# Optimization experiments

Hardware: AMD Instinct MI355X
Metric: run time of the kernel (lower is better)

Reference implementation:

```python
import jax, jax.numpy as jnp
import numpy as np

DEPTH, SRC, TRG, B, H = 2, 32, 32, 64, 256


def setup_inputs() -> dict:
    key = jax.random.key(0)
    k0, k1, k2, k3 = jax.random.split(key, 4)
    return {
        "src": jax.random.normal(k0, (SRC, B, H), jnp.float32),
        "trg": jax.random.normal(k1, (TRG, B, H), jnp.float32),
        # xavier-normal-ish scaling for the recurrent / input weights
        "W": jax.random.normal(k2, (DEPTH, H, H), jnp.float32) * (1.0 / np.sqrt(H)),
        "U": jax.random.normal(k3, (DEPTH, 2 * H, H), jnp.float32) * (1.0 / np.sqrt(2 * H)),
        "b": jnp.zeros((DEPTH, H), jnp.float32),
    }


def _run_depth(xw, yw, U, b):
    """2D grid recurrence for one depth.
    xw, yw: [SRC, TRG, B, H] precomputed input projections (x_t @ W, y_t @ W).
    Returns hx, hy: [SRC, TRG, B, H].
    Note: both top and left recurrent states come from the h_x channel,
    matching h_output[d][i-1][j][0] and h_output[d][i][j-1][0] in the source.
    """
    h = b.shape[0]
    U_top, U_left = U[:h], U[h:]  # state = concat([state_x, state_y], dim=1)

    def row_step(top_row, row_in):
        # top_row: [TRG, B, H] = h_x of row i-1
        xw_i, yw_i = row_in  # each [TRG, B, H]

        def col_step(left_hx, cell_in):
            xw_t, yw_t, top_hx = cell_in  # each [B, H]
            rec = top_hx @ U_top + left_hx @ U_left + b
            h_x = jnp.tanh(xw_t + rec)
            h_y = jnp.tanh(yw_t + rec)
            return h_x, (h_x, h_y)

        _, (hx_row, hy_row) = jax.lax.scan(
            col_step, jnp.zeros_like(top_row[0]), (xw_i, yw_i, top_row))
        return hx_row, (hx_row, hy_row)

    top0 = jnp.zeros_like(xw[0])  # state_x = 0 when i == 0
    _, (hx, hy) = jax.lax.scan(row_step, top0, (xw, yw))
    return hx, hy


def reference(src, trg, W, U, b):
    depth = W.shape[0]
    src_len, batch, hidden = src.shape
    trg_len = trg.shape[0]
    # depth-0 inputs: x_t = src[i], y_t = trg[j] broadcast over the grid
    xg = jnp.broadcast_to(src[:, None], (src_len, trg_len, batch, hidden))
    yg = jnp.broadcast_to(trg[None, :], (src_len, trg_len, batch, hidden))
    outs = []
    for d in range(depth):
        xw = jnp.einsum('ijbh,hk->ijbk', xg, W[d])
        yw = jnp.einsum('ijbh,hk->ijbk', yg, W[d])
        hx, hy = _run_depth(xw, yw, U[d], b[d])
        outs.append(jnp.stack([hx, hy], axis=2))  # [SRC, TRG, 2, B, H]
        xg, yg = hx, hy  # next depth consumes h_output[d-1][i][j][0/1]
    return jnp.stack(outs, axis=0)  # [depth, SRC, TRG, 2, B, H]
```

## Files before the change

### kernel.cpp

```cpp
#include <hip/hip_runtime.h>
#include <math.h>

#define S 32
#define T 32
#define B 64
#define H 256
#define MSZ 65536
#define ROWSP 16

typedef __attribute__((ext_vector_type(8))) short s16x8;
typedef __attribute__((ext_vector_type(4))) float f32x4;

__device__ inline unsigned short f2b(float f){
    unsigned u = __builtin_bit_cast(unsigned, f);
    u += 0x7fffu + ((u >> 16) & 1u);
    return (unsigned short)(u >> 16);
}
__device__ inline float b2f(unsigned short s){
    unsigned u = ((unsigned)s) << 16;
    return __builtin_bit_cast(float, u);
}
__device__ inline float tanh_fast(float x){
    float e = __builtin_amdgcn_exp2f(x * 2.8853900817779268f);
    float r = __builtin_amdgcn_rcpf(e + 1.0f);
    return fmaf(-2.0f, r, 1.0f);
}
__device__ inline void waitflag(int* f, int target){
    while (__hip_atomic_load(f, __ATOMIC_RELAXED, __HIP_MEMORY_SCOPE_AGENT) < target)
        __builtin_amdgcn_s_sleep(2);
    (void)__hip_atomic_load(f, __ATOMIC_ACQUIRE, __HIP_MEMORY_SCOPE_AGENT);
}

__global__ __launch_bounds__(256) void prep_kernel(
    const float* __restrict__ U, const float* __restrict__ W,
    unsigned short* __restrict__ Bsw)
{
    int t = blockIdx.x * 256 + threadIdx.x;
    if (t >= 5 * MSZ) return;
    int m  = t >> 16;
    int r  = t & 65535;
    int kt = r >> 13;
    int r2 = r & 8191;
    int c  = r2 >> 5;
    int kk = r2 & 31;
    int krow = kt * 32 + kk;
    float v;
    if (m < 4){ int d = m >> 1, ope = m & 1; v = U[((size_t)d*2*H + ope*H + krow)*H + c]; }
    else      { v = W[((size_t)H + krow)*H + c]; }
    Bsw[t] = f2b(v);
}

__global__ __launch_bounds__(256) void proj0b_kernel(
    const float* __restrict__ src, const float* __restrict__ trg,
    const float* __restrict__ W0, unsigned short* __restrict__ sxw,
    unsigned short* __restrict__ tyw)
{
    const int c = threadIdx.x;
    int gr0 = blockIdx.x * ROWSP;
    const float* inp; unsigned short* outp; int r0;
    if (gr0 < S * B) { inp = src; outp = sxw; r0 = gr0; }
    else             { inp = trg; outp = tyw; r0 = gr0 - S * B; }

    float acc[ROWSP];
#pragma unroll
    for (int rr = 0; rr < ROWSP; ++rr) acc[rr] = 0.f;
    for (int k = 0; k < H; ++k) {
        float wv = W0[k * H + c];
#pragma unroll
        for (int rr = 0; rr < ROWSP; ++rr)
            acc[rr] = fmaf(inp[(size_t)(r0 + rr) * H + k], wv, acc[rr]);
    }
#pragma unroll
    for (int rr = 0; rr < ROWSP; ++rr)
        outp[(size_t)(r0 + rr) * H + c] = f2b(acc[rr]);
}

__global__ __launch_bounds__(256) void zeroflags_kernel(int* flags, int n){
    int t = blockIdx.x * 256 + threadIdx.x;
    if (t < n) flags[t] = 0;
}

__global__ __launch_bounds__(512, 2) void grid_kernel(
    const unsigned short* __restrict__ Bsw,
    const unsigned short* __restrict__ sxwb,
    const unsigned short* __restrict__ tywb,
    const float* __restrict__ bvec,
    float* __restrict__ out,
    int* __restrict__ flags)
{
    __shared__ unsigned short Alds[4 * 64 * 128];
    char* AldsB = (char*)Alds;

    const int blk   = blockIdx.x;
    const int depth = blk >> 6;
    const int i     = (blk & 63) >> 1;
    const int half  = blk & 1;
    const int c0    = half * 128;

    const int tid  = threadIdx.x;
    const int lane = tid & 63;
    const int wv   = tid >> 6;
    const int colq = lane & 15;
    const int hi   = lane >> 4;
    const int kk0  = hi * 8;
    const int col  = c0 + wv * 16 + colq;
    const int hi16 = hi * 16;
    const int lswz = (colq & 7) << 4;

    const int row64 = tid >> 3;
    const int k4b   = (tid & 7) * 4;
    const int swz   = (row64 & 7) << 4;

    int* flag0 = flags;
    int* flag1 = flags + S * T;

    s16x8 bfT[8], bfL[8], bfW[8];
    {
        const unsigned short* mT = Bsw + (size_t)(depth == 0 ? 0 : 2) * MSZ;
        const unsigned short* mL = Bsw + (size_t)(depth == 0 ? 1 : 3) * MSZ;
        const unsigned short* mW = Bsw + (size_t)4 * MSZ;
#pragma unroll
        for (int kt = 0; kt < 8; ++kt) {
            int o = (kt * H + col) * 32 + kk0;
            bfT[kt] = *(const s16x8*)(mT + o);
            bfL[kt] = *(const s16x8*)(mL + o);
            bfW[kt] = *(const s16x8*)(mW + o);
        }
    }

    const size_t CH = (size_t)B * H;
#define OPTR(dd,ii,jj,ch) (out + ((((size_t)(dd)*S + (ii))*T + (jj))*2 + (ch)) * CH)

#define LOADOP(OP, SP, KC) do { \
    const float* _p = (SP) + (size_t)row64 * H + (KC)*128 + k4b*4; \
    L[(OP)*4+0] = *(const float4*)(_p); \
    L[(OP)*4+1] = *(const float4*)(_p + 4); \
    L[(OP)*4+2] = *(const float4*)(_p + 8); \
    L[(OP)*4+3] = *(const float4*)(_p + 12); \
} while(0)

#define WRITEOP(OP) do { \
    _Pragma("unroll") \
    for (int _l = 0; _l < 4; ++_l) { \
        float4 _v = L[(OP)*4+_l]; \
        uint2 _u; \
        _u.x = f2b(_v.x) | ((unsigned)f2b(_v.y) << 16); \
        _u.y = f2b(_v.z) | ((unsigned)f2b(_v.w) << 16); \
        *(uint2*)(AldsB + (OP)*16384 + row64*256 + (((k4b+_l)*8) ^ swz)) = _u; \
    } \
} while(0)

#define AFRAG(OP, RT, KTL) (*(const s16x8*)(AldsB + (OP)*16384 + ((RT)*16 + colq)*256 + ((((KTL)*64) + hi16) ^ lswz)))

#define OPPHASE(OP, FP, TGT, SPTR, BF, ACC) do { \
    if ((FP)) { if (tid == 0) waitflag((FP), (TGT)); } \
    __syncthreads(); \
    const float* _sp = (SPTR); \
    LOADOP(OP, _sp, 0); \
    WRITEOP(OP); \
    __syncthreads(); \
    LOADOP(OP, _sp, 1); \
    _Pragma("unroll") \
    for (int _ktl = 0; _ktl < 4; ++_ktl) \
        _Pragma("unroll") \
        for (int _rt = 0; _rt < 4; ++_rt) \
            ACC[_rt] = __builtin_amdgcn_mfma_f32_16x16x32_bf16(AFRAG(OP,_rt,_ktl), BF[_ktl], ACC[_rt], 0, 0, 0); \
    __syncthreads(); \
    WRITEOP(OP); \
    __syncthreads(); \
    _Pragma("unroll") \
    for (int _ktl = 0; _ktl < 4; ++_ktl) \
        _Pragma("unroll") \
        for (int _rt = 0; _rt < 4; ++_rt) \
            ACC[_rt] = __builtin_amdgcn_mfma_f32_16x16x32_bf16(AFRAG(OP,_rt,_ktl), BF[4+_ktl], ACC[_rt], 0, 0, 0); \
} while(0)

    if (depth == 0) {
        unsigned short xwr[16];
        {
            const unsigned short* xwp = sxwb + (size_t)i * B * H;
#pragma unroll
            for (int rt = 0; rt < 4; ++rt)
#pragma unroll
                for (int q = 0; q < 4; ++q)
                    xwr[rt*4+q] = xwp[(size_t)(rt*16 + hi*4 + q) * H + col];
        }

        for (int j = 0; j < T; ++j) {
            unsigned short ywr[16];
            {
                const unsigned short* ywp = tywb + (size_t)j * B * H;
#pragma unroll
                for (int rt = 0; rt < 4; ++rt)
#pragma unroll
                    for (int q = 0; q < 4; ++q)
                        ywr[rt*4+q] = ywp[(size_t)(rt*16 + hi*4 + q) * H + col];
            }

            f32x4 acc[4];
#pragma unroll
            for (int rt = 0; rt < 4; ++rt) acc[rt] = (f32x4)(0.f);
            float4 L[16];

            if (j > 0)
                OPPHASE(1, &flag0[i*T + (j-1)], 2, OPTR(0, i, j-1, 0), bfL, acc);
            if (i > 0)
                OPPHASE(0, &flag0[(i-1)*T + j], 2, OPTR(0, i-1, j, 0), bfT, acc);

            float* ox = OPTR(0, i, j, 0);
            float* oy = OPTR(0, i, j, 1);
            const float bc = bvec[col];
#pragma unroll
            for (int rt = 0; rt < 4; ++rt)
#pragma unroll
                for (int q = 0; q < 4; ++q) {
                    int idx = rt*4 + q;
                    int row = rt*16 + hi*4 + q;
                    float rec = acc[rt][q] + bc;
                    float hx = tanh_fast(b2f(xwr[idx]) + rec);
                    float hy = tanh_fast(b2f(ywr[idx]) + rec);
                    __hip_atomic_store(&ox[row*H + col], hx, __ATOMIC_RELAXED, __HIP_MEMORY_SCOPE_AGENT);
                    __hip_atomic_store(&oy[row*H + col], hy, __ATOMIC_RELAXED, __HIP_MEMORY_SCOPE_AGENT);
                }

            asm volatile("s_waitcnt vmcnt(0)" ::: "memory");
            __syncthreads();
            if (tid == 0)
                __hip_atomic_fetch_add(&flag0[i*T + j], 1, __ATOMIC_RELEASE, __HIP_MEMORY_SCOPE_AGENT);
        }
    } else {
        for (int j = 0; j < T; ++j) {
            f32x4 ar[4], ax[4], ay[4];
#pragma unroll
            for (int rt = 0; rt < 4; ++rt){ ar[rt] = (f32x4)(0.f); ax[rt] = (f32x4)(0.f); ay[rt] = (f32x4)(0.f); }
            float4 L[16];

            {
                if (tid == 0) waitflag(&flag0[i*T + j], 2);
                __syncthreads();
                const float* sHx0 = OPTR(0, i, j, 0);
                const float* sHy0 = OPTR(0, i, j, 1);
                LOADOP(2, sHx0, 0); LOADOP(3, sHy0, 0);
                WRITEOP(2); WRITEOP(3);
                __syncthreads();
                LOADOP(2, sHx0, 1); LOADOP(3, sHy0, 1);
#pragma unroll
                for (int ktl = 0; ktl < 4; ++ktl)
#pragma unroll
                    for (int rt = 0; rt < 4; ++rt) {
                        ax[rt] = __builtin_amdgcn_mfma_f32_16x16x32_bf16(AFRAG(2,rt,ktl), bfW[ktl], ax[rt], 0, 0, 0);
                        ay[rt] = __builtin_amdgcn_mfma_f32_16x16x32_bf16(AFRAG(3,rt,ktl), bfW[ktl], ay[rt], 0, 0, 0);
                    }
                __syncthreads();
                WRITEOP(2); WRITEOP(3);
                __syncthreads();
#pragma unroll
                for (int ktl = 0; ktl < 4; ++ktl)
#pragma unroll
                    for (int rt = 0; rt < 4; ++rt) {
                        ax[rt] = __builtin_amdgcn_mfma_f32_16x16x32_bf16(AFRAG(2,rt,ktl), bfW[4+ktl], ax[rt], 0, 0, 0);
                        ay[rt] = __builtin_amdgcn_mfma_f32_16x16x32_bf16(AFRAG(3,rt,ktl), bfW[4+ktl], ay[rt], 0, 0, 0);
                    }
            }

            if (j > 0)
                OPPHASE(1, &flag1[i*T + (j-1)], 2, OPTR(1, i, j-1, 0), bfL, ar);
            if (i > 0)
                OPPHASE(0, &flag1[(i-1)*T + j], 2, OPTR(1, i-1, j, 0), bfT, ar);

            float recs[16];
            float* ox = OPTR(1, i, j, 0);
            const float bc = bvec[H + col];
#pragma unroll
            for (int rt = 0; rt < 4; ++rt)
#pragma unroll
                for (int q = 0; q < 4; ++q) {
                    int idx = rt*4 + q;
                    int row = rt*16 + hi*4 + q;
                    float rec = ar[rt][q] + bc;
                    recs[idx] = rec;
                    float hx = tanh_fast(ax[rt][q] + rec);
                    __hip_atomic_store(&ox[row*H + col], hx, __ATOMIC_RELAXED, __HIP_MEMORY_SCOPE_AGENT);
                }
            asm volatile("s_waitcnt vmcnt(0)" ::: "memory");
            __syncthreads();
            if (tid == 0)
                __hip_atomic_fetch_add(&flag1[i*T + j], 1, __ATOMIC_RELEASE, __HIP_MEMORY_SCOPE_AGENT);

            float* oy = OPTR(1, i, j, 1);
#pragma unroll
            for (int rt = 0; rt < 4; ++rt)
#pragma unroll
                for (int q = 0; q < 4; ++q) {
                    int idx = rt*4 + q;
                    int row = rt*16 + hi*4 + q;
                    float hy = tanh_fast(ay[rt][q] + recs[idx]);
                    __hip_atomic_store(&oy[row*H + col], hy, __ATOMIC_RELAXED, __HIP_MEMORY_SCOPE_AGENT);
                }
        }
    }
#undef OPTR
#undef LOADOP
#undef WRITEOP
#undef AFRAG
#undef OPPHASE
}

__device__ inline s16x8 make_afrag(const float* __restrict__ M, int arow, int k0){
    const float* p = M + arow * H + k0;
    float4 x = *(const float4*)(p);
    float4 y = *(const float4*)(p + 4);
    s16x8 r;
    r[0]=(short)f2b(x.x); r[1]=(short)f2b(x.y); r[2]=(short)f2b(x.z); r[3]=(short)f2b(x.w);
    r[4]=(short)f2b(y.x); r[5]=(short)f2b(y.y); r[6]=(short)f2b(y.z); r[7]=(short)f2b(y.w);
    return r;
}

__global__ __launch_bounds__(64) void stage_kernel(
    const unsigned short* __restrict__ Bsw,
    const unsigned short* __restrict__ sxwb,
    const unsigned short* __restrict__ tywb,
    const float* __restrict__ bvec,
    float* __restrict__ out, int v)
{
    const int lane = threadIdx.x;
    const int cellid = blockIdx.x >> 2;
    const int stripe = blockIdx.x & 3;

    int ilo0 = (v > T-1) ? v-(T-1) : 0, ihi0 = (v < S-1) ? v : S-1;
    int n0 = (v <= S+T-2) ? (ihi0 - ilo0 + 1) : 0;
    if (n0 < 0) n0 = 0;
    int w1 = v - 1;
    int ilo1 = (w1 > T-1) ? w1-(T-1) : 0;

    int d, i, j;
    if (cellid < n0) { d = 0; i = ilo0 + cellid; j = v - i; }
    else             { d = 1; int q = cellid - n0; i = ilo1 + q; j = w1 - i; }

    const int r0   = stripe * 16;
    const int arow = r0 + (lane & 15);
    const int kk0  = (lane >> 4) * 8;
    const int colq = lane & 15;
    const int rowq = r0 + ((lane >> 4) << 2);

#define OUTB(dd,ii,jj,ch) (out + ((((size_t)(dd)*S + (ii))*T + (jj))*2 + (ch)) * (size_t)(B*H))

    if (d == 0) {
        f32x4 acc[16];
#pragma unroll
        for (int t = 0; t < 16; ++t) acc[t] = (f32x4)(0.f);
        if (i > 0) {
            const float* topM = OUTB(0, i-1, j, 0);
            const unsigned short* Bt = Bsw + 0*MSZ;
            for (int kt = 0; kt < 8; ++kt) {
                s16x8 a = make_afrag(topM, arow, kt*32 + kk0);
                const unsigned short* bp = Bt + (kt*H + colq)*32 + kk0;
#pragma unroll
                for (int ct = 0; ct < 16; ++ct)
                    acc[ct] = __builtin_amdgcn_mfma_f32_16x16x32_bf16(a, *(const s16x8*)(bp + ct*512), acc[ct], 0, 0, 0);
            }
        }
        if (j > 0) {
            const float* lftM = OUTB(0, i, j-1, 0);
            const unsigned short* Bl = Bsw + 1*MSZ;
            for (int kt = 0; kt < 8; ++kt) {
                s16x8 a = make_afrag(lftM, arow, kt*32 + kk0);
                const unsigned short* bp = Bl + (kt*H + colq)*32 + kk0;
#pragma unroll
                for (int ct = 0; ct < 16; ++ct)
                    acc[ct] = __builtin_amdgcn_mfma_f32_16x16x32_bf16(a, *(const s16x8*)(bp + ct*512), acc[ct], 0, 0, 0);
            }
        }
        const unsigned short* xwp = sxwb + (size_t)i * B * H;
        const unsigned short* ywp = tywb + (size_t)j * B * H;
        float* ox = OUTB(0, i, j, 0);
        float* oy = OUTB(0, i, j, 1);
#pragma unroll
        for (int ct = 0; ct < 16; ++ct) {
            int col = ct*16 + colq;
            float bc = bvec[col];
#pragma unroll
            for (int q = 0; q < 4; ++q) {
                int row = rowq + q;
                float rec = acc[ct][q] + bc;
                ox[row*H + col] = tanh_fast(b2f(xwp[row*H + col]) + rec);
                oy[row*H + col] = tanh_fast(b2f(ywp[row*H + col]) + rec);
            }
        }
    } else {
        const float* hx0 = OUTB(0, i, j, 0);
        const float* hy0 = OUTB(0, i, j, 1);
        const float* topM = (i > 0) ? OUTB(1, i-1, j, 0) : (const float*)0;
        const float* lftM = (j > 0) ? OUTB(1, i, j-1, 0) : (const float*)0;
        const unsigned short* BU1t = Bsw + 2*MSZ;
        const unsigned short* BU1l = Bsw + 3*MSZ;
        const unsigned short* BW1  = Bsw + 4*MSZ;
        float* ox = OUTB(1, i, j, 0);
        float* oy = OUTB(1, i, j, 1);

        for (int halfc = 0; halfc < 2; ++halfc) {
            f32x4 arr[8], axx[8], ayy[8];
#pragma unroll
            for (int t = 0; t < 8; ++t) { arr[t]=(f32x4)(0.f); axx[t]=(f32x4)(0.f); ayy[t]=(f32x4)(0.f); }
            const int bbase = halfc*4096 + colq*32 + kk0;

            for (int kt = 0; kt < 8; ++kt) {
                const int k0 = kt*32 + kk0;
                const int bofs = kt*H*32 + bbase;
                if (topM) {
                    s16x8 a = make_afrag(topM, arow, k0);
#pragma unroll
                    for (int ct = 0; ct < 8; ++ct)
                        arr[ct] = __builtin_amdgcn_mfma_f32_16x16x32_bf16(a, *(const s16x8*)(BU1t + bofs + ct*512), arr[ct], 0, 0, 0);
                }
                if (lftM) {
                    s16x8 a = make_afrag(lftM, arow, k0);
#pragma unroll
                    for (int ct = 0; ct < 8; ++ct)
                        arr[ct] = __builtin_amdgcn_mfma_f32_16x16x32_bf16(a, *(const s16x8*)(BU1l + bofs + ct*512), arr[ct], 0, 0, 0);
                }
                {
                    s16x8 a = make_afrag(hx0, arow, k0);
#pragma unroll
                    for (int ct = 0; ct < 8; ++ct)
                        axx[ct] = __builtin_amdgcn_mfma_f32_16x16x32_bf16(a, *(const s16x8*)(BW1 + bofs + ct*512), axx[ct], 0, 0, 0);
                }
                {
                    s16x8 a = make_afrag(hy0, arow, k0);
#pragma unroll
                    for (int ct = 0; ct < 8; ++ct)
                        ayy[ct] = __builtin_amdgcn_mfma_f32_16x16x32_bf16(a, *(const s16x8*)(BW1 + bofs + ct*512), ayy[ct], 0, 0, 0);
                }
            }
#pragma unroll
            for (int ct = 0; ct < 8; ++ct) {
                int col = halfc*128 + ct*16 + colq;
                float bc = bvec[H + col];
#pragma unroll
                for (int q = 0; q < 4; ++q) {
                    int row = rowq + q;
                    float rec = arr[ct][q] + bc;
                    ox[row*H + col] = tanh_fast(axx[ct][q] + rec);
                    oy[row*H + col] = tanh_fast(ayy[ct][q] + rec);
                }
            }
        }
    }
#undef OUTB
}

extern "C" void kernel_launch(void* const* d_in, const int* in_sizes, int n_in,
                              void* d_out, int out_size, void* d_ws, size_t ws_size,
                              hipStream_t stream)
{
    const float* src = (const float*)d_in[0];
    const float* trg = (const float*)d_in[1];
    const float* W   = (const float*)d_in[2];
    const float* U   = (const float*)d_in[3];
    const float* b   = (const float*)d_in[4];
    float* out = (float*)d_out;

    const size_t need_stage   = (size_t)5*MSZ*2 + (size_t)2*S*B*H*2;
    const size_t need_persist = need_stage + (size_t)2*S*T*sizeof(int);

    unsigned short* Bsw  = (unsigned short*)d_ws;
    unsigned short* sxwb = Bsw + (size_t)5*MSZ;
    unsigned short* tywb = sxwb + (size_t)S*B*H;
    int* flags = (int*)(tywb + (size_t)S*B*H);

    if (ws_size >= need_persist) {
        prep_kernel<<<(5*MSZ + 255)/256, 256, 0, stream>>>(U, W, Bsw);
        proj0b_kernel<<<2*S*B/ROWSP, 256, 0, stream>>>(src, trg, W, sxwb, tywb);
        zeroflags_kernel<<<(2*S*T + 255)/256, 256, 0, stream>>>(flags, 2*S*T);
        grid_kernel<<<128, 512, 0, stream>>>(Bsw, sxwb, tywb, b, out, flags);
        return;
    }

    prep_kernel<<<(5*MSZ + 255)/256, 256, 0, stream>>>(U, W, Bsw);
    proj0b_kernel<<<2*S*B/ROWSP, 256, 0, stream>>>(src, trg, W, sxwb, tywb);
    for (int v = 0; v < S + T; ++v) {
        int ilo0 = (v > T-1) ? v-(T-1) : 0, ihi0 = (v < S-1) ? v : S-1;
        int n0 = (v <= S+T-2) ? (ihi0 - ilo0 + 1) : 0;
        if (n0 < 0) n0 = 0;
        int n1 = 0;
        int w1 = v - 1;
        if (w1 >= 0) {
            int ilo1 = (w1 > T-1) ? w1-(T-1) : 0, ihi1 = (w1 < S-1) ? w1 : S-1;
            n1 = ihi1 - ilo1 + 1;
        }
        stage_kernel<<<4*(n0+n1), 64, 0, stream>>>(Bsw, sxwb, tywb, b, out, v);
    }
}
```

Measured before the change: 672.4 us.

## Split depth-1 input projection into dedicated producer blocks feeding via flags

Adds a third group of 64 blocks that computes the depth-1 input projections (h0 @ W) for each cell and stages them in the depth-1 output slots, signalling through a new flag array. The depth-1 recurrence blocks then only load those precomputed values and run the U matmuls, which takes the W matmul off their sequential critical path. The cost is an extra global round trip, the extra flags, and 192 persistent blocks instead of 128, which must all be co-resident to avoid deadlock.

```diff
diff --git a/kernel.cpp b/kernel.cpp
--- a/kernel.cpp
+++ b/kernel.cpp
@@ -92,7 +92,7 @@
     char* AldsB = (char*)Alds;
 
     const int blk   = blockIdx.x;
-    const int depth = blk >> 6;
+    const int btyp  = blk >> 6;
     const int i     = (blk & 63) >> 1;
     const int half  = blk & 1;
     const int c0    = half * 128;
@@ -113,20 +113,7 @@
 
     int* flag0 = flags;
     int* flag1 = flags + S * T;
-
-    s16x8 bfT[8], bfL[8], bfW[8];
-    {
-        const unsigned short* mT = Bsw + (size_t)(depth == 0 ? 0 : 2) * MSZ;
-        const unsigned short* mL = Bsw + (size_t)(depth == 0 ? 1 : 3) * MSZ;
-        const unsigned short* mW = Bsw + (size_t)4 * MSZ;
-#pragma unroll
-        for (int kt = 0; kt < 8; ++kt) {
-            int o = (kt * H + col) * 32 + kk0;
-            bfT[kt] = *(const s16x8*)(mT + o);
-            bfL[kt] = *(const s16x8*)(mL + o);
-            bfW[kt] = *(const s16x8*)(mW + o);
-        }
-    }
+    int* flagg = flags + 2 * S * T;
 
     const size_t CH = (size_t)B * H;
 #define OPTR(dd,ii,jj,ch) (out + ((((size_t)(dd)*S + (ii))*T + (jj))*2 + (ch)) * CH)
@@ -175,7 +162,14 @@
             ACC[_rt] = __builtin_amdgcn_mfma_f32_16x16x32_bf16(AFRAG(OP,_rt,_ktl), BF[4+_ktl], ACC[_rt], 0, 0, 0); \
 } while(0)
 
-    if (depth == 0) {
+    if (btyp == 0) {
+        s16x8 bfT[8], bfL[8];
+#pragma unroll
+        for (int kt = 0; kt < 8; ++kt) {
+            int o = (kt * H + col) * 32 + kk0;
+            bfT[kt] = *(const s16x8*)(Bsw + o);
+            bfL[kt] = *(const s16x8*)(Bsw + (size_t)MSZ + o);
+        }
         unsigned short xwr[16];
         {
             const unsigned short* xwp = sxwb + (size_t)i * B * H;
@@ -228,40 +222,37 @@
             if (tid == 0)
                 __hip_atomic_fetch_add(&flag0[i*T + j], 1, __ATOMIC_RELEASE, __HIP_MEMORY_SCOPE_AGENT);
         }
-    } else {
+    } else if (btyp == 1) {
+        s16x8 bfT[8], bfL[8];
+#pragma unroll
+        for (int kt = 0; kt < 8; ++kt) {
+            int o = (kt * H + col) * 32 + kk0;
+            bfT[kt] = *(const s16x8*)(Bsw + (size_t)2*MSZ + o);
+            bfL[kt] = *(const s16x8*)(Bsw + (size_t)3*MSZ + o);
+        }
+
         for (int j = 0; j < T; ++j) {
-            f32x4 ar[4], ax[4], ay[4];
-#pragma unroll
-            for (int rt = 0; rt < 4; ++rt){ ar[rt] = (f32x4)(0.f); ax[rt] = (f32x4)(0.f); ay[rt] = (f32x4)(0.f); }
+            if (tid == 0) waitflag(&flagg[i*T + j], 2);
+            __syncthreads();
+            float pxr[16], pyr[16];
+            {
+                const float* p0s = OPTR(1, i, j, 0);
+                const float* p1s = OPTR(1, i, j, 1);
+#pragma unroll
+                for (int rt = 0; rt < 4; ++rt)
+#pragma unroll
+                    for (int q = 0; q < 4; ++q) {
+                        int idx = rt*4 + q;
+                        int row = rt*16 + hi*4 + q;
+                        pxr[idx] = p0s[row*H + col];
+                        pyr[idx] = p1s[row*H + col];
+                    }
+            }
+
+            f32x4 ar[4];
+#pragma unroll
+            for (int rt = 0; rt < 4; ++rt) ar[rt] = (f32x4)(0.f);
             float4 L[16];
-
-            {
-                if (tid == 0) waitflag(&flag0[i*T + j], 2);
-                __syncthreads();
-                const float* sHx0 = OPTR(0, i, j, 0);
-                const float* sHy0 = OPTR(0, i, j, 1);
-                LOADOP(2, sHx0, 0); LOADOP(3, sHy0, 0);
-                WRITEOP(2); WRITEOP(3);
-                __syncthreads();
-                LOADOP(2, sHx0, 1); LOADOP(3, sHy0, 1);
-#pragma unroll
-                for (int ktl = 0; ktl < 4; ++ktl)
-#pragma unroll
-                    for (int rt = 0; rt < 4; ++rt) {
-                        ax[rt] = __builtin_amdgcn_mfma_f32_16x16x32_bf16(AFRAG(2,rt,ktl), bfW[ktl], ax[rt], 0, 0, 0);
-                        ay[rt] = __builtin_amdgcn_mfma_f32_16x16x32_bf16(AFRAG(3,rt,ktl), bfW[ktl], ay[rt], 0, 0, 0);
-                    }
-                __syncthreads();
-                WRITEOP(2); WRITEOP(3);
-                __syncthreads();
-#pragma unroll
-                for (int ktl = 0; ktl < 4; ++ktl)
-#pragma unroll
-                    for (int rt = 0; rt < 4; ++rt) {
-                        ax[rt] = __builtin_amdgcn_mfma_f32_16x16x32_bf16(AFRAG(2,rt,ktl), bfW[4+ktl], ax[rt], 0, 0, 0);
-                        ay[rt] = __builtin_amdgcn_mfma_f32_16x16x32_bf16(AFRAG(3,rt,ktl), bfW[4+ktl], ay[rt], 0, 0, 0);
-                    }
-            }
 
             if (j > 0)
                 OPPHASE(1, &flag1[i*T + (j-1)], 2, OPTR(1, i, j-1, 0), bfL, ar);
@@ -279,7 +270,7 @@
                     int row = rt*16 + hi*4 + q;
                     float rec = ar[rt][q] + bc;
                     recs[idx] = rec;
-                    float hx = tanh_fast(ax[rt][q] + rec);
+                    float hx = tanh_fast(pxr[idx] + rec);
                     __hip_atomic_store(&ox[row*H + col], hx, __ATOMIC_RELAXED, __HIP_MEMORY_SCOPE_AGENT);
                 }
             asm volatile("s_waitcnt vmcnt(0)" ::: "memory");
@@ -294,9 +285,63 @@
                 for (int q = 0; q < 4; ++q) {
                     int idx = rt*4 + q;
                     int row = rt*16 + hi*4 + q;
-                    float hy = tanh_fast(ay[rt][q] + recs[idx]);
+                    float hy = tanh_fast(pyr[idx] + recs[idx]);
                     __hip_atomic_store(&oy[row*H + col], hy, __ATOMIC_RELAXED, __HIP_MEMORY_SCOPE_AGENT);
                 }
+        }
+    } else {
+        s16x8 bfW[8];
+#pragma unroll
+        for (int kt = 0; kt < 8; ++kt)
+            bfW[kt] = *(const s16x8*)(Bsw + (size_t)4*MSZ + (kt * H + col) * 32 + kk0);
+
+        for (int j = 0; j < T; ++j) {
+            if (tid == 0) waitflag(&flag0[i*T + j], 2);
+            __syncthreads();
+
+            f32x4 px[4], py[4];
+#pragma unroll
+            for (int rt = 0; rt < 4; ++rt) { px[rt] = (f32x4)(0.f); py[rt] = (f32x4)(0.f); }
+            float4 L[16];
+
+            const float* sHx0 = OPTR(0, i, j, 0);
+            const float* sHy0 = OPTR(0, i, j, 1);
+            LOADOP(2, sHx0, 0); LOADOP(3, sHy0, 0);
+            WRITEOP(2); WRITEOP(3);
+            __syncthreads();
+            LOADOP(2, sHx0, 1); LOADOP(3, sHy0, 1);
+#pragma unroll
+            for (int ktl = 0; ktl < 4; ++ktl)
+#pragma unroll
+                for (int rt = 0; rt < 4; ++rt) {
+                    px[rt] = __builtin_amdgcn_mfma_f32_16x16x32_bf16(AFRAG(2,rt,ktl), bfW[ktl], px[rt], 0, 0, 0);
+                    py[rt] = __builtin_amdgcn_mfma_f32_16x16x32_bf16(AFRAG(3,rt,ktl), bfW[ktl], py[rt], 0, 0, 0);
+                }
+            __syncthreads();
+            WRITEOP(2); WRITEOP(3);
+            __syncthreads();
+#pragma unroll
+            for (int ktl = 0; ktl < 4; ++ktl)
+#pragma unroll
+                for (int rt = 0; rt < 4; ++rt) {
+                    px[rt] = __builtin_amdgcn_mfma_f32_16x16x32_bf16(AFRAG(2,rt,ktl), bfW[4+ktl], px[rt], 0, 0, 0);
+                    py[rt] = __builtin_amdgcn_mfma_f32_16x16x32_bf16(AFRAG(3,rt,ktl), bfW[4+ktl], py[rt], 0, 0, 0);
+                }
+
+            float* p0 = OPTR(1, i, j, 0);
+            float* p1 = OPTR(1, i, j, 1);
+#pragma unroll
+            for (int rt = 0; rt < 4; ++rt)
+#pragma unroll
+                for (int q = 0; q < 4; ++q) {
+                    int row = rt*16 + hi*4 + q;
+                    __hip_atomic_store(&p0[row*H + col], px[rt][q], __ATOMIC_RELAXED, __HIP_MEMORY_SCOPE_AGENT);
+                    __hip_atomic_store(&p1[row*H + col], py[rt][q], __ATOMIC_RELAXED, __HIP_MEMORY_SCOPE_AGENT);
+                }
+            asm volatile("s_waitcnt vmcnt(0)" ::: "memory");
+            __syncthreads();
+            if (tid == 0)
+                __hip_atomic_fetch_add(&flagg[i*T + j], 1, __ATOMIC_RELEASE, __HIP_MEMORY_SCOPE_AGENT);
         }
     }
 #undef OPTR
@@ -460,8 +505,9 @@
     const float* b   = (const float*)d_in[4];
     float* out = (float*)d_out;
 
+    const int nflags = 3 * S * T;
     const size_t need_stage   = (size_t)5*MSZ*2 + (size_t)2*S*B*H*2;
-    const size_t need_persist = need_stage + (size_t)2*S*T*sizeof(int);
+    const size_t need_persist = need_stage + (size_t)nflags*sizeof(int);
 
     unsigned short* Bsw  = (unsigned short*)d_ws;
     unsigned short* sxwb = Bsw + (size_t)5*MSZ;
@@ -471,8 +517,8 @@
     if (ws_size >= need_persist) {
         prep_kernel<<<(5*MSZ + 255)/256, 256, 0, stream>>>(U, W, Bsw);
         proj0b_kernel<<<2*S*B/ROWSP, 256, 0, stream>>>(src, trg, W, sxwb, tywb);
-        zeroflags_kernel<<<(2*S*T + 255)/256, 256, 0, stream>>>(flags, 2*S*T);
-        grid_kernel<<<128, 512, 0, stream>>>(Bsw, sxwb, tywb, b, out, flags);
+        zeroflags_kernel<<<(nflags + 255)/256, 256, 0, stream>>>(flags, nflags);
+        grid_kernel<<<192, 512, 0, stream>>>(Bsw, sxwb, tywb, b, out, flags);
         return;
     }
 
```

After: 641.3 us. -4.6%, faster.
